# Kernel tuning notes

Hardware: AMD Instinct MI355X
Metric: run time of the kernel (lower is better)

Reference implementation:

```python
import jax, jax.numpy as jnp
import numpy as np

H = 256       # hiddenDim
E = 300       # embDim
VOCAB = 50000
S = 1024      # number of sentences in document
L = 64        # words per sentence (chain-tree depth)
TOPIC = 100
TARGET = 5


def setup_inputs() -> dict:
    key = jax.random.key(0)
    ks = jax.random.split(key, 21)
    f32 = jnp.float32
    return {
        'sentenceInIndex': jax.random.randint(ks[0], (S, L), 0, VOCAB),
        'depTypes': jax.random.randint(ks[1], (S, L - 1), 0, 9),
        'D_T_distr': jax.random.uniform(ks[2], (TOPIC,), dtype=f32),
        'h0': jax.random.normal(ks[3], (H,), dtype=f32),
        'idx2vec': jax.random.normal(ks[4], (VOCAB, E), dtype=f32) * 0.1,
        'q': jax.random.normal(ks[5], (10, H), dtype=f32) * 0.1,
        'W': jax.random.normal(ks[6], (3 * H, E), dtype=f32) * 0.05,
        'U': jax.random.normal(ks[7], (3 * H, H), dtype=f32) * 0.05,
        'D': jax.random.normal(ks[8], (3 * H, H), dtype=f32) * 0.05,
        'b': jax.random.normal(ks[9], (3 * H,), dtype=f32) * 0.05,
        'gru_wih': jax.random.normal(ks[10], (3 * H, H), dtype=f32) * 0.05,
        'gru_whh': jax.random.normal(ks[11], (3 * H, H), dtype=f32) * 0.05,
        'gru_bih': jax.random.normal(ks[12], (3 * H,), dtype=f32) * 0.05,
        'gru_bhh': jax.random.normal(ks[13], (3 * H,), dtype=f32) * 0.05,
        'gate_W': jax.random.normal(ks[14], (2 * H, H), dtype=f32) * 0.05,
        'gate_U': jax.random.normal(ks[15], (2 * H, H), dtype=f32) * 0.05,
        'gate_b': jax.random.normal(ks[16], (2 * H,), dtype=f32) * 0.05,
        'mlp_W': jax.random.normal(ks[17], (H, TOPIC), dtype=f32) * 0.05,
        'mlp_b': jax.random.normal(ks[18], (H,), dtype=f32) * 0.05,
        'out_W': jax.random.normal(ks[19], (TARGET, H), dtype=f32) * 0.05,
        'out_b': jax.random.normal(ks[20], (TARGET,), dtype=f32) * 0.05,
    }


def reference(sentenceInIndex, depTypes, D_T_distr, h0, idx2vec, q, W, U, D, b,
              gru_wih, gru_whh, gru_bih, gru_bhh,
              gate_W, gate_U, gate_b, mlp_W, mlp_b, out_W, out_b):
    # ---- DERNN over chain-canonicalized dependency trees (vectorized over S sentences) ----
    x = idx2vec[sentenceInIndex]                        # [S, L, E] gather
    Wx = jnp.einsum('sle,ke->slk', x, W)                # [S, L, 3H]
    qe = q[depTypes]                                    # [S, L-1, H] dep-type embeddings for edges k->k+1
    Dq = jnp.einsum('slh,kh->slk', qe, D)               # [S, L-1, 3H]

    # leaf node (position L-1): q_sum = q[-1] ('leafNotion'); no child h term
    dq_leaf = D @ q[-1]                                 # [3H]
    iu_leaf = Wx[:, -1, H:] + dq_leaf[H:] + b[H:]       # [S, 2H]
    h = jnp.tanh(jax.nn.sigmoid(iu_leaf[:, :H]) * jnp.tanh(iu_leaf[:, H:]))  # [S, H]

    # internal nodes k = L-2 .. 0, single child k+1 (edge k)
    pre = Wx[:, :L - 1] + Dq + b                        # [S, L-1, 3H]
    pre_rev = jnp.swapaxes(pre[:, ::-1], 0, 1)          # [L-1, S, 3H] bottom-up order

    def tree_step(h_c, pre_k):
        tot = pre_k + h_c @ U.T                         # [S, 3H]
        f = jax.nn.sigmoid(tot[:, :H]) * h_c            # child forget gate * child h (single child => sum)
        i = jax.nn.sigmoid(tot[:, H:2 * H])
        u = jnp.tanh(tot[:, 2 * H:])
        h_n = jnp.tanh(i * u + f)
        return h_n, None

    sentenceVector, _ = jax.lax.scan(tree_step, h, pre_rev)  # [S, H] root hidden per sentence

    # ---- GRU over sentence sequence (batch 1), torch nn.GRU math ----
    def gru_step(hh, xt):
        gi = gru_wih @ xt + gru_bih                     # [3H]
        gh = gru_whh @ hh + gru_bhh
        r = jax.nn.sigmoid(gi[:H] + gh[:H])
        z = jax.nn.sigmoid(gi[H:2 * H] + gh[H:2 * H])
        n = jnp.tanh(gi[2 * H:] + r * gh[2 * H:])
        return (1.0 - z) * n + z * hh, None

    hT, _ = jax.lax.scan(gru_step, h0, sentenceVector)  # [H] final hidden state

    # ---- topic vector, GATE fusion, classifier ----
    t = jnp.tanh(mlp_W @ D_T_distr + mlp_b)             # [H]
    g = gate_W @ hT + gate_U @ t + gate_b               # [2H]
    v = jnp.tanh(jax.nn.sigmoid(g[:H]) * hT + jax.nn.sigmoid(g[H:]) * t)
    return jax.nn.softmax(out_W @ v + out_b)            # [TARGET]
```

## Files before the change

kernel.cpp:

```cpp
#include <hip/hip_runtime.h>

typedef short short8 __attribute__((ext_vector_type(8)));
typedef float f4 __attribute__((ext_vector_type(4)));
typedef int i4 __attribute__((ext_vector_type(4)));
typedef _Float16 half8 __attribute__((ext_vector_type(8)));
typedef _Float16 h2 __attribute__((ext_vector_type(2)));

#define HD 256
#define ED 300
#define EP 320
#define TH 768
#define NS 1024
#define LW 64
#define SH 4.5f

__device__ __forceinline__ unsigned short f2bf(float f) {
    unsigned int u = __float_as_uint(f);
    u = (u + 0x7FFFu + ((u >> 16) & 1u)) >> 16;
    return (unsigned short)u;
}
__device__ __forceinline__ float bf2f(unsigned short s) {
    return __uint_as_float(((unsigned int)s) << 16);
}
__device__ __forceinline__ float sigm(float x) {
    return __builtin_amdgcn_rcpf(1.f + __expf(-x));
}
__device__ __forceinline__ float tanh_(float x) {
    x = fminf(fmaxf(x, -15.f), 15.f);
    return 1.f - 2.f * __builtin_amdgcn_rcpf(1.f + __expf(2.f * x));
}
__device__ __forceinline__ unsigned int pack_h2(float a, float b) {
    h2 p; p.x = (_Float16)a; p.y = (_Float16)b;
    return __builtin_bit_cast(unsigned int, p);
}

__device__ __forceinline__ void load8bf(const unsigned short* p, float* o) {
    uint4 a = *(const uint4*)p;
    o[0] = bf2f((unsigned short)(a.x & 0xffff)); o[1] = bf2f((unsigned short)(a.x >> 16));
    o[2] = bf2f((unsigned short)(a.y & 0xffff)); o[3] = bf2f((unsigned short)(a.y >> 16));
    o[4] = bf2f((unsigned short)(a.z & 0xffff)); o[5] = bf2f((unsigned short)(a.z >> 16));
    o[6] = bf2f((unsigned short)(a.w & 0xffff)); o[7] = bf2f((unsigned short)(a.w >> 16));
}
__device__ __forceinline__ void ubf4(uint2 a, float* o) {
    o[0] = bf2f((unsigned short)(a.x & 0xffff)); o[1] = bf2f((unsigned short)(a.x >> 16));
    o[2] = bf2f((unsigned short)(a.y & 0xffff)); o[3] = bf2f((unsigned short)(a.y >> 16));
}

__global__ void k_prep(const float* __restrict__ W, const float* __restrict__ U,
                       const float* __restrict__ Wih, const float* __restrict__ Whh,
                       const float* __restrict__ q, const float* __restrict__ Dm,
                       const float* __restrict__ DT, const float* __restrict__ mlpW,
                       const float* __restrict__ mlpb,
                       const float* __restrict__ bih, const float* __restrict__ bhh,
                       unsigned short* __restrict__ Wb, _Float16* __restrict__ Uh,
                       _Float16* __restrict__ Wihh,
                       signed char* __restrict__ Wq, float* __restrict__ rowscale,
                       float* __restrict__ bias2,
                       float* __restrict__ Dq, float* __restrict__ tv) {
    __shared__ float smax[4];
    int bid = blockIdx.x, tid = threadIdx.x;
    if (bid < 768) {
        int r = bid;
        for (int j = tid; j < EP; j += 256)
            Wb[r * EP + j] = (j < ED) ? f2bf(W[r * ED + j]) : (unsigned short)0;
        float whv = Whh[r * HD + tid];
        for (int j = tid; j < HD; j += 256) {
            Uh[r * HD + j] = (_Float16)U[r * HD + j];
            Wihh[r * HD + j] = (_Float16)Wih[r * HD + j];
        }
        float v = fabsf(whv);
        for (int o = 32; o; o >>= 1) v = fmaxf(v, __shfl_xor(v, o));
        if ((tid & 63) == 0) smax[tid >> 6] = v;
        __syncthreads();
        float am = fmaxf(fmaxf(smax[0], smax[1]), fmaxf(smax[2], smax[3]));
        float inv = (am > 0.f) ? 127.f / am : 0.f;
        int qi = (int)rintf(whv * inv);
        qi = max(-127, min(127, qi));
        Wq[r * HD + tid] = (signed char)qi;
        if (tid == 0) rowscale[r] = (am / 127.f) * (SH / 127.f);
    } else if (bid < 798) {
        int idx = bid - 768;
        int d = idx / 3, part = idx - d * 3;
        int n = part * 256 + tid;
        float s = 0.f;
        for (int h = 0; h < HD; ++h) s += Dm[n * HD + h] * q[d * HD + h];
        Dq[d * TH + n] = s;
    } else {
        if (tid < HD) {
            float s = 0.f;
            for (int k = 0; k < 100; ++k) s += mlpW[tid * 100 + k] * DT[k];
            tv[tid] = tanh_(s + mlpb[tid]);
        }
        for (int r = tid; r < TH; r += 256)
            bias2[r] = bih[r] + ((r < 512) ? bhh[r] : 0.f);
    }
}

#define XP 328
__launch_bounds__(256, 2)
__global__ void k_phaseB(const int* __restrict__ sIdx, const int* __restrict__ depT,
                         const float* __restrict__ emb, const unsigned short* __restrict__ Wb,
                         const float* __restrict__ Dq, const float* __restrict__ bias,
                         unsigned short* __restrict__ pre) {
    __shared__ float dq_s[10 * 772];
    __shared__ float b_s[TH];
    __shared__ int dep_s[32];
    __shared__ int idx_s[32];
    __shared__ __align__(16) unsigned short xbf[32 * XP];
    __shared__ __align__(16) unsigned short tbuf[16 * 776];
    int tid = threadIdx.x;
    int c0 = blockIdx.x * 32;
    for (int i = tid; i < 10 * 768; i += 256) {
        int d = i / 768, n = i - d * 768;
        dq_s[d * 772 + n] = Dq[i];
    }
    for (int i = tid; i < TH; i += 256) b_s[i] = bias[i];
    if (tid < 32) {
        int m = c0 + tid;
        idx_s[tid] = sIdx[m];
        int l = m & 63, s = m >> 6;
        dep_s[tid] = (l == 63) ? 9 : depT[s * 63 + l];
    }
    __syncthreads();
    for (int i = tid; i < 32 * EP; i += 256) {
        int row = i / EP, col = i - row * EP;
        unsigned short v = 0;
        if (col < ED) v = f2bf(emb[(long)idx_s[row] * ED + col]);
        xbf[row * XP + col] = v;
    }
    __syncthreads();

    int lane = tid & 63;
    int w = tid >> 6;
    int quad = lane >> 4, l16 = lane & 15;

    f4 acc[2][12];
#pragma unroll
    for (int cs = 0; cs < 2; ++cs)
#pragma unroll
        for (int ms = 0; ms < 12; ++ms) acc[cs][ms] = (f4){0.f, 0.f, 0.f, 0.f};

    const unsigned short* wbase = Wb + (w * 192 + l16) * EP;

#pragma unroll
    for (int kt = 0; kt < 10; ++kt) {
        int k0 = kt * 32 + quad * 8;
        short8 bf0 = *(const short8*)&xbf[l16 * XP + k0];
        short8 bf1 = *(const short8*)&xbf[(16 + l16) * XP + k0];
#pragma unroll
        for (int ms = 0; ms < 12; ++ms) {
            short8 af = *(const short8*)(wbase + ms * 16 * EP + k0);
            acc[0][ms] = __builtin_amdgcn_mfma_f32_16x16x32_bf16(af, bf0, acc[0][ms], 0, 0, 0);
            acc[1][ms] = __builtin_amdgcn_mfma_f32_16x16x32_bf16(af, bf1, acc[1][ms], 0, 0, 0);
        }
    }

#pragma unroll
    for (int cs = 0; cs < 2; ++cs) {
        int dep = dep_s[cs * 16 + l16];
#pragma unroll
        for (int ms = 0; ms < 12; ++ms) {
            int ncol = w * 192 + ms * 16 + quad * 4;
            f4 dq4 = *(const f4*)&dq_s[dep * 772 + ncol];
            f4 b4 = *(const f4*)&b_s[ncol];
            unsigned int lo = (unsigned int)f2bf(acc[cs][ms][0] + dq4[0] + b4[0]) |
                              ((unsigned int)f2bf(acc[cs][ms][1] + dq4[1] + b4[1]) << 16);
            unsigned int hi = (unsigned int)f2bf(acc[cs][ms][2] + dq4[2] + b4[2]) |
                              ((unsigned int)f2bf(acc[cs][ms][3] + dq4[3] + b4[3]) << 16);
            uint2 v; v.x = lo; v.y = hi;
            *(uint2*)&tbuf[l16 * 776 + ncol] = v;
        }
        __syncthreads();
        for (int it = 0; it < 6; ++it) {
            int flat = it * 256 + tid;
            int row = flat / 96;
            int ch = flat - row * 96;
            uint4 v = *(const uint4*)&tbuf[row * 776 + ch * 8];
            *(uint4*)(pre + (long)(c0 + cs * 16 + row) * TH + ch * 8) = v;
        }
        __syncthreads();
    }
}

__global__ void __launch_bounds__(768) k_phaseC(
                         const unsigned short* __restrict__ pre,
                         const _Float16* __restrict__ Uh,
                         const _Float16* __restrict__ Wihh,
                         const float* __restrict__ bias2,
                         float* __restrict__ gi) {
    __shared__ __align__(16) uint4 hfr[512];
    __shared__ __align__(16) float tot[16 * 772];
    int tid = threadIdx.x;
    int lane = tid & 63, w = tid >> 6, quad = lane >> 4, l16 = lane & 15;
    int s0 = blockIdx.x * 16;

    uint4 frag[32];
    {
        const _Float16* base = Uh + (w * 64 + l16) * HD;
#pragma unroll
        for (int t = 0; t < 4; ++t)
#pragma unroll
            for (int kt = 0; kt < 8; ++kt)
                frag[t * 8 + kt] = *(const uint4*)(base + t * 16 * HD + kt * 32 + quad * 8);
    }

    int us = tid >> 5;
    int jg = tid & 31;
    int j0 = jg * 8;
    int hcell = (j0 >> 5) * 64 + 16 * ((j0 >> 3) & 3) + us;
    uint4 hcp;

    if (tid < 512) {
        const unsigned short* prow = pre + ((long)(s0 + us) * LW + 63) * TH;
        float iv[8], uv[8], hcv[8];
        load8bf(prow + 256 + j0, iv);
        load8bf(prow + 512 + j0, uv);
#pragma unroll
        for (int r = 0; r < 8; ++r) hcv[r] = tanh_(sigm(iv[r]) * tanh_(uv[r]));
        hcp.x = pack_h2(hcv[0], hcv[1]); hcp.y = pack_h2(hcv[2], hcv[3]);
        hcp.z = pack_h2(hcv[4], hcv[5]); hcp.w = pack_h2(hcv[6], hcv[7]);
        hfr[hcell] = hcp;
    }
    __syncthreads();

    int mb = w * 64 + quad * 4;

    for (int step = 0; step < 63; ++step) {
        int l = 62 - step;
        uint2 praw[6];
        if (tid < 512) {
            const unsigned short* prow = pre + ((long)(s0 + us) * LW + l) * TH;
#pragma unroll
            for (int g = 0; g < 3; ++g) {
                praw[2 * g]     = *(const uint2*)(prow + g * 256 + j0);
                praw[2 * g + 1] = *(const uint2*)(prow + g * 256 + j0 + 4);
            }
        }
        f4 a0 = (f4){0,0,0,0}, a1 = (f4){0,0,0,0}, a2 = (f4){0,0,0,0}, a3 = (f4){0,0,0,0};
#pragma unroll
        for (int kt = 0; kt < 8; ++kt) {
            half8 b = __builtin_bit_cast(half8, hfr[kt * 64 + lane]);
            a0 = __builtin_amdgcn_mfma_f32_16x16x32_f16(__builtin_bit_cast(half8, frag[kt]), b, a0, 0, 0, 0);
            a1 = __builtin_amdgcn_mfma_f32_16x16x32_f16(__builtin_bit_cast(half8, frag[8 + kt]), b, a1, 0, 0, 0);
            a2 = __builtin_amdgcn_mfma_f32_16x16x32_f16(__builtin_bit_cast(half8, frag[16 + kt]), b, a2, 0, 0, 0);
            a3 = __builtin_amdgcn_mfma_f32_16x16x32_f16(__builtin_bit_cast(half8, frag[24 + kt]), b, a3, 0, 0, 0);
        }
        float* tr = tot + l16 * 772;
        *(f4*)&tr[mb] = a0;
        *(f4*)&tr[mb + 16] = a1;
        *(f4*)&tr[mb + 32] = a2;
        *(f4*)&tr[mb + 48] = a3;
        __syncthreads();
        if (tid < 512) {
            const float* ts = tot + us * 772;
            float hcv[8];
            h2 px = __builtin_bit_cast(h2, hcp.x); h2 py = __builtin_bit_cast(h2, hcp.y);
            h2 pz = __builtin_bit_cast(h2, hcp.z); h2 pw = __builtin_bit_cast(h2, hcp.w);
            hcv[0] = (float)px.x; hcv[1] = (float)px.y; hcv[2] = (float)py.x; hcv[3] = (float)py.y;
            hcv[4] = (float)pz.x; hcv[5] = (float)pz.y; hcv[6] = (float)pw.x; hcv[7] = (float)pw.y;
#pragma unroll
            for (int hf = 0; hf < 2; ++hf) {
                int jb = j0 + hf * 4;
                float pf[4], pi_[4], pu[4];
                ubf4(praw[hf], pf);
                ubf4(praw[2 + hf], pi_);
                ubf4(praw[4 + hf], pu);
                f4 tf = *(const f4*)&ts[jb];
                f4 ti = *(const f4*)&ts[256 + jb];
                f4 tu = *(const f4*)&ts[512 + jb];
#pragma unroll
                for (int r = 0; r < 4; ++r) {
                    float ff = tf[r] + pf[r];
                    float ii = ti[r] + pi_[r];
                    float uu = tu[r] + pu[r];
                    hcv[hf * 4 + r] = tanh_(sigm(ii) * tanh_(uu) + sigm(ff) * hcv[hf * 4 + r]);
                }
            }
            hcp.x = pack_h2(hcv[0], hcv[1]); hcp.y = pack_h2(hcv[2], hcv[3]);
            hcp.z = pack_h2(hcv[4], hcv[5]); hcp.w = pack_h2(hcv[6], hcv[7]);
            hfr[hcell] = hcp;
        }
        __syncthreads();
    }

    {
        const _Float16* base = Wihh + (w * 64 + l16) * HD;
#pragma unroll
        for (int t = 0; t < 4; ++t)
#pragma unroll
            for (int kt = 0; kt < 8; ++kt)
                frag[t * 8 + kt] = *(const uint4*)(base + t * 16 * HD + kt * 32 + quad * 8);
    }
    f4 a0 = (f4){0,0,0,0}, a1 = (f4){0,0,0,0}, a2 = (f4){0,0,0,0}, a3 = (f4){0,0,0,0};
#pragma unroll
    for (int kt = 0; kt < 8; ++kt) {
        half8 b = __builtin_bit_cast(half8, hfr[kt * 64 + lane]);
        a0 = __builtin_amdgcn_mfma_f32_16x16x32_f16(__builtin_bit_cast(half8, frag[kt]), b, a0, 0, 0, 0);
        a1 = __builtin_amdgcn_mfma_f32_16x16x32_f16(__builtin_bit_cast(half8, frag[8 + kt]), b, a1, 0, 0, 0);
        a2 = __builtin_amdgcn_mfma_f32_16x16x32_f16(__builtin_bit_cast(half8, frag[16 + kt]), b, a2, 0, 0, 0);
        a3 = __builtin_amdgcn_mfma_f32_16x16x32_f16(__builtin_bit_cast(half8, frag[24 + kt]), b, a3, 0, 0, 0);
    }
    float* go = gi + (long)(s0 + l16) * TH;
    f4 b0 = *(const f4*)(bias2 + mb);
    f4 b1 = *(const f4*)(bias2 + mb + 16);
    f4 b2 = *(const f4*)(bias2 + mb + 32);
    f4 b3 = *(const f4*)(bias2 + mb + 48);
    *(f4*)(go + mb) = a0 + b0;
    *(f4*)(go + mb + 16) = a1 + b1;
    *(f4*)(go + mb + 32) = a2 + b2;
    *(f4*)(go + mb + 48) = a3 + b3;
}

#define GB 8
__global__ void __launch_bounds__(512) k_gru(
                      const signed char* __restrict__ Wq, const float* __restrict__ rowscale,
                      const float* __restrict__ bhh,
                      const float* __restrict__ gi, const float* __restrict__ h0,
                      const float* __restrict__ tv,
                      const float* __restrict__ gateW, const float* __restrict__ gateU,
                      const float* __restrict__ gateb,
                      const float* __restrict__ outW, const float* __restrict__ outb,
                      float* __restrict__ out) {
    __shared__ __align__(16) signed char qbuf[2][HD];
    __shared__ __align__(16) float gbuf[2][GB * TH];
    __shared__ float hts[HD];
    __shared__ float sgs[512];
    __shared__ float vvs[HD];
    __shared__ float lg[8];

    int tid = threadIdx.x;
    int lane = tid & 63, w = tid >> 6, quad = lane >> 4, l16 = lane & 15;

    i4 far_[2][4], faz[2][4], fan[2][4];
#pragma unroll
    for (int c = 0; c < 2; ++c) {
        const signed char* qr_ = Wq + (long)(w * 32 + c * 16 + l16) * HD;
        const signed char* qz_ = Wq + (long)(256 + w * 32 + c * 16 + l16) * HD;
        const signed char* qn_ = Wq + (long)(512 + w * 32 + c * 16 + l16) * HD;
#pragma unroll
        for (int kc = 0; kc < 4; ++kc) {
            far_[c][kc] = *(const i4*)(qr_ + kc * 64 + quad * 16);
            faz[c][kc] = *(const i4*)(qz_ + kc * 64 + quad * 16);
            fan[c][kc] = *(const i4*)(qn_ + kc * 64 + quad * 16);
        }
    }

    int sc = (l16 >> 2) & 1;
    int sr = l16 & 3;
    int j = w * 32 + sc * 16 + quad * 4 + sr;
    bool b2 = (sr & 2) != 0, b1 = (sr & 1) != 0, bc = (sc != 0);
    bool owner = (l16 < 8);

    float rs_r = rowscale[j];
    float rs_z = rowscale[256 + j];
    float rs_n = rowscale[512 + j];
    float bn_l = bhh[512 + j];

    float hv = h0[j];
    if (owner) {
        float hc = fminf(fmaxf(hv, -SH), SH);
        qbuf[0][j] = (signed char)(int)rintf(hc * (127.f / SH));
    }
    float rg[12];
#pragma unroll
    for (int i = 0; i < 12; ++i) gbuf[0][i * 512 + tid] = gi[i * 512 + tid];
#pragma unroll
    for (int i = 0; i < 12; ++i) rg[i] = gi[GB * TH + i * 512 + tid];
    __syncthreads();

    for (int nb = 0; nb < NS / GB; ++nb) {
        int buf = nb & 1;
#pragma unroll
        for (int u = 0; u < GB; ++u) {
            if (u == 0) {
#pragma unroll
                for (int i = 0; i < 12; ++i) gbuf[buf ^ 1][i * 512 + tid] = rg[i];
                if (nb + 2 < NS / GB) {
                    const float* gsrc = gi + (long)(nb + 2) * GB * TH;
#pragma unroll
                    for (int i = 0; i < 12; ++i) rg[i] = gsrc[i * 512 + tid];
                }
            }
            const int p = u & 1;
            const float* gl = &gbuf[buf][u * TH];
            float gr_l = gl[j], gz_l = gl[256 + j], gn_l = gl[512 + j];

            i4 qr[2], qz[2], qn[2];
#pragma unroll
            for (int c = 0; c < 2; ++c) { qr[c] = (i4){0,0,0,0}; qz[c] = (i4){0,0,0,0}; qn[c] = (i4){0,0,0,0}; }
#pragma unroll
            for (int kc = 0; kc < 4; ++kc) {
                i4 b = *(const i4*)&qbuf[p][kc * 64 + quad * 16];
                qr[0] = __builtin_amdgcn_mfma_i32_16x16x64_i8(far_[0][kc], b, qr[0], 0, 0, 0);
                qr[1] = __builtin_amdgcn_mfma_i32_16x16x64_i8(far_[1][kc], b, qr[1], 0, 0, 0);
                qz[0] = __builtin_amdgcn_mfma_i32_16x16x64_i8(faz[0][kc], b, qz[0], 0, 0, 0);
                qz[1] = __builtin_amdgcn_mfma_i32_16x16x64_i8(faz[1][kc], b, qz[1], 0, 0, 0);
                qn[0] = __builtin_amdgcn_mfma_i32_16x16x64_i8(fan[0][kc], b, qn[0], 0, 0, 0);
                qn[1] = __builtin_amdgcn_mfma_i32_16x16x64_i8(fan[1][kc], b, qn[1], 0, 0, 0);
            }
            int ra0 = bc ? qr[1][0] : qr[0][0], ra1 = bc ? qr[1][1] : qr[0][1];
            int ra2 = bc ? qr[1][2] : qr[0][2], ra3 = bc ? qr[1][3] : qr[0][3];
            int rt0 = b2 ? ra2 : ra0, rt1 = b2 ? ra3 : ra1;
            int qrv = b1 ? rt1 : rt0;
            int za0 = bc ? qz[1][0] : qz[0][0], za1 = bc ? qz[1][1] : qz[0][1];
            int za2 = bc ? qz[1][2] : qz[0][2], za3 = bc ? qz[1][3] : qz[0][3];
            int zt0 = b2 ? za2 : za0, zt1 = b2 ? za3 : za1;
            int qzv = b1 ? zt1 : zt0;
            int na0 = bc ? qn[1][0] : qn[0][0], na1 = bc ? qn[1][1] : qn[0][1];
            int na2 = bc ? qn[1][2] : qn[0][2], na3 = bc ? qn[1][3] : qn[0][3];
            int nt0 = b2 ? na2 : na0, nt1 = b2 ? na3 : na1;
            int qnv = b1 ? nt1 : nt0;
            float rv = sigm(gr_l + (float)qrv * rs_r);
            float zv = sigm(gz_l + (float)qzv * rs_z);
            float nv = tanh_(gn_l + rv * ((float)qnv * rs_n + bn_l));
            hv = (1.f - zv) * nv + zv * hv;
            if (owner) {
                float hc = fminf(fmaxf(hv, -SH), SH);
                qbuf[p ^ 1][j] = (signed char)(int)rintf(hc * (127.f / SH));
            }
            __syncthreads();
        }
    }

    if (owner) hts[j] = hv;
    __syncthreads();
    {
        float s = gateb[tid];
        for (int k = 0; k < HD; ++k)
            s += gateW[tid * HD + k] * hts[k] + gateU[tid * HD + k] * tv[k];
        sgs[tid] = sigm(s);
    }
    __syncthreads();
    if (tid < HD) vvs[tid] = tanh_(sgs[tid] * hts[tid] + sgs[256 + tid] * tv[tid]);
    __syncthreads();
    if (tid < 5) {
        float s = outb[tid];
        for (int k = 0; k < HD; ++k) s += outW[tid * HD + k] * vvs[k];
        lg[tid] = s;
    }
    __syncthreads();
    if (tid == 0) {
        float m = lg[0];
        for (int i = 1; i < 5; ++i) m = fmaxf(m, lg[i]);
        float e[5], sum = 0.f;
        for (int i = 0; i < 5; ++i) { e[i] = __expf(lg[i] - m); sum += e[i]; }
        for (int i = 0; i < 5; ++i) out[i] = e[i] / sum;
    }
}

extern "C" void kernel_launch(void* const* d_in, const int* in_sizes, int n_in,
                              void* d_out, int out_size, void* d_ws, size_t ws_size,
                              hipStream_t stream) {
    (void)in_sizes; (void)n_in; (void)out_size; (void)ws_size;
    const int* sIdx = (const int*)d_in[0];
    const int* depT = (const int*)d_in[1];
    const float* DT = (const float*)d_in[2];
    const float* h0 = (const float*)d_in[3];
    const float* emb = (const float*)d_in[4];
    const float* q = (const float*)d_in[5];
    const float* W = (const float*)d_in[6];
    const float* U = (const float*)d_in[7];
    const float* Dm = (const float*)d_in[8];
    const float* b = (const float*)d_in[9];
    const float* Wih = (const float*)d_in[10];
    const float* Whh = (const float*)d_in[11];
    const float* bih = (const float*)d_in[12];
    const float* bhh = (const float*)d_in[13];
    const float* gateW = (const float*)d_in[14];
    const float* gateU = (const float*)d_in[15];
    const float* gateb = (const float*)d_in[16];
    const float* mlpW = (const float*)d_in[17];
    const float* mlpb = (const float*)d_in[18];
    const float* outW = (const float*)d_in[19];
    const float* outb = (const float*)d_in[20];

    char* ws = (char*)d_ws;
    unsigned short* Wb = (unsigned short*)ws;   ws += 768 * 320 * 2;
    _Float16* Uh = (_Float16*)ws;               ws += 768 * 256 * 2;
    _Float16* Wihh = (_Float16*)ws;             ws += 768 * 256 * 2;
    signed char* Wq = (signed char*)ws;         ws += 768 * 256;
    float* rowscale = (float*)ws;               ws += 768 * 4;
    float* bias2 = (float*)ws;                  ws += 768 * 4;
    float* Dq = (float*)ws;                     ws += 10 * 768 * 4;
    float* tv = (float*)ws;                     ws += 1024;
    ws = (char*)d_ws + ((((size_t)(ws - (char*)d_ws)) + 4095) & ~(size_t)4095);
    unsigned short* pre = (unsigned short*)ws;  ws += (size_t)65536 * 768 * 2;
    float* gi = (float*)ws;                     ws += (size_t)1024 * 768 * 4;

    k_prep<<<dim3(799), dim3(256), 0, stream>>>(W, U, Wih, Whh, q, Dm, DT, mlpW, mlpb,
                                                bih, bhh,
                                                Wb, Uh, Wihh, Wq, rowscale, bias2, Dq, tv);
    k_phaseB<<<dim3(2048), dim3(256), 0, stream>>>(sIdx, depT, emb, Wb, Dq, b, pre);
    k_phaseC<<<dim3(64), dim3(768), 0, stream>>>(pre, Uh, Wihh, bias2, gi);
    k_gru<<<dim3(1), dim3(512), 0, stream>>>(Wq, rowscale, bhh, gi, h0, tv,
                                             gateW, gateU, gateb, outW, outb, (float*)d_out);
}
```

Baseline: 1.207 ms.

## Pin GRU int8 weights in AGPRs via inline asm and split GRU launch

The recurrent int8 weight fragments are moved into accumulation registers, and the MFMA is issued through inline asm with AGPR operands. This is meant to cut VGPR pressure and avoid spills or register copies in the serial GRU loop. The 1024-step GRU is also split into two single-block launches of 512 steps each, with the hidden state passed through global memory. That adds launch overhead and still runs strictly serially. A bug remains: the prefetch guard `nb+2 < NS/GB` still reads `gi` past the first half's boundary, which is harmless but wasteful.

After: 1.357 ms. +12.4%, slower.

```diff
diff --git a/kernel.cpp b/kernel.cpp
--- a/kernel.cpp
+++ b/kernel.cpp
@@ -44,6 +44,16 @@
 __device__ __forceinline__ void ubf4(uint2 a, float* o) {
     o[0] = bf2f((unsigned short)(a.x & 0xffff)); o[1] = bf2f((unsigned short)(a.x >> 16));
     o[2] = bf2f((unsigned short)(a.y & 0xffff)); o[3] = bf2f((unsigned short)(a.y >> 16));
+}
+
+__device__ __forceinline__ i4 to_a(i4 v) {
+    i4 r;
+    asm("" : "=a"(r) : "0"(v));
+    return r;
+}
+__device__ __forceinline__ void mfma_i8_acc(i4& acc, i4 a, i4 b) {
+    asm volatile("v_mfma_i32_16x16x64_i8 %0, %1, %2, %0"
+                 : "+a"(acc) : "a"(a), "v"(b));
 }
 
 __global__ void k_prep(const float* __restrict__ W, const float* __restrict__ U,
@@ -320,7 +330,8 @@
                       const float* __restrict__ gateW, const float* __restrict__ gateU,
                       const float* __restrict__ gateb,
                       const float* __restrict__ outW, const float* __restrict__ outb,
-                      float* __restrict__ out) {
+                      float* __restrict__ out,
+                      float* __restrict__ hstate, int t0, int do_head) {
     __shared__ __align__(16) signed char qbuf[2][HD];
     __shared__ __align__(16) float gbuf[2][GB * TH];
     __shared__ float hts[HD];
@@ -339,9 +350,9 @@
         const signed char* qn_ = Wq + (long)(512 + w * 32 + c * 16 + l16) * HD;
 #pragma unroll
         for (int kc = 0; kc < 4; ++kc) {
-            far_[c][kc] = *(const i4*)(qr_ + kc * 64 + quad * 16);
-            faz[c][kc] = *(const i4*)(qz_ + kc * 64 + quad * 16);
-            fan[c][kc] = *(const i4*)(qn_ + kc * 64 + quad * 16);
+            far_[c][kc] = to_a(*(const i4*)(qr_ + kc * 64 + quad * 16));
+            faz[c][kc] = to_a(*(const i4*)(qz_ + kc * 64 + quad * 16));
+            fan[c][kc] = to_a(*(const i4*)(qn_ + kc * 64 + quad * 16));
         }
     }
 
@@ -356,20 +367,26 @@
     float rs_n = rowscale[512 + j];
     float bn_l = bhh[512 + j];
 
-    float hv = h0[j];
+    float hv = (t0 == 0) ? h0[j] : hstate[j];
     if (owner) {
         float hc = fminf(fmaxf(hv, -SH), SH);
         qbuf[0][j] = (signed char)(int)rintf(hc * (127.f / SH));
     }
+    const int nb0 = t0 / GB;
     float rg[12];
-#pragma unroll
-    for (int i = 0; i < 12; ++i) gbuf[0][i * 512 + tid] = gi[i * 512 + tid];
-#pragma unroll
-    for (int i = 0; i < 12; ++i) rg[i] = gi[GB * TH + i * 512 + tid];
-    __syncthreads();
-
-    for (int nb = 0; nb < NS / GB; ++nb) {
-        int buf = nb & 1;
+    {
+        const float* g0 = gi + (long)nb0 * GB * TH;
+        const float* g1 = gi + (long)(nb0 + 1) * GB * TH;
+#pragma unroll
+        for (int i = 0; i < 12; ++i) gbuf[0][i * 512 + tid] = g0[i * 512 + tid];
+#pragma unroll
+        for (int i = 0; i < 12; ++i) rg[i] = g1[i * 512 + tid];
+    }
+    __syncthreads();
+
+    for (int nbr = 0; nbr < 512 / GB; ++nbr) {
+        int nb = nb0 + nbr;
+        int buf = nbr & 1;
 #pragma unroll
         for (int u = 0; u < GB; ++u) {
             if (u == 0) {
@@ -391,12 +408,12 @@
 #pragma unroll
             for (int kc = 0; kc < 4; ++kc) {
                 i4 b = *(const i4*)&qbuf[p][kc * 64 + quad * 16];
-                qr[0] = __builtin_amdgcn_mfma_i32_16x16x64_i8(far_[0][kc], b, qr[0], 0, 0, 0);
-                qr[1] = __builtin_amdgcn_mfma_i32_16x16x64_i8(far_[1][kc], b, qr[1], 0, 0, 0);
-                qz[0] = __builtin_amdgcn_mfma_i32_16x16x64_i8(faz[0][kc], b, qz[0], 0, 0, 0);
-                qz[1] = __builtin_amdgcn_mfma_i32_16x16x64_i8(faz[1][kc], b, qz[1], 0, 0, 0);
-                qn[0] = __builtin_amdgcn_mfma_i32_16x16x64_i8(fan[0][kc], b, qn[0], 0, 0, 0);
-                qn[1] = __builtin_amdgcn_mfma_i32_16x16x64_i8(fan[1][kc], b, qn[1], 0, 0, 0);
+                mfma_i8_acc(qr[0], far_[0][kc], b);
+                mfma_i8_acc(qr[1], far_[1][kc], b);
+                mfma_i8_acc(qz[0], faz[0][kc], b);
+                mfma_i8_acc(qz[1], faz[1][kc], b);
+                mfma_i8_acc(qn[0], fan[0][kc], b);
+                mfma_i8_acc(qn[1], fan[1][kc], b);
             }
             int ra0 = bc ? qr[1][0] : qr[0][0], ra1 = bc ? qr[1][1] : qr[0][1];
             int ra2 = bc ? qr[1][2] : qr[0][2], ra3 = bc ? qr[1][3] : qr[0][3];
@@ -420,6 +437,11 @@
             }
             __syncthreads();
         }
+    }
+
+    if (!do_head) {
+        if (owner) hstate[j] = hv;
+        return;
     }
 
     if (owner) hts[j] = hv;
@@ -483,6 +505,7 @@
     float* bias2 = (float*)ws;                  ws += 768 * 4;
     float* Dq = (float*)ws;                     ws += 10 * 768 * 4;
     float* tv = (float*)ws;                     ws += 1024;
+    float* hstate = (float*)ws;                 ws += 1024;
     ws = (char*)d_ws + ((((size_t)(ws - (char*)d_ws)) + 4095) & ~(size_t)4095);
     unsigned short* pre = (unsigned short*)ws;  ws += (size_t)65536 * 768 * 2;
     float* gi = (float*)ws;                     ws += (size_t)1024 * 768 * 4;
@@ -493,5 +516,9 @@
     k_phaseB<<<dim3(2048), dim3(256), 0, stream>>>(sIdx, depT, emb, Wb, Dq, b, pre);
     k_phaseC<<<dim3(64), dim3(768), 0, stream>>>(pre, Uh, Wihh, bias2, gi);
     k_gru<<<dim3(1), dim3(512), 0, stream>>>(Wq, rowscale, bhh, gi, h0, tv,
-                                             gateW, gateU, gateb, outW, outb, (float*)d_out);
-}
+                                             gateW, gateU, gateb, outW, outb, (float*)d_out,
+                                             hstate, 0, 0);
+    k_gru<<<dim3(1), dim3(512), 0, stream>>>(Wq, rowscale, bhh, gi, h0, tv,
+                                             gateW, gateU, gateb, outW, outb, (float*)d_out,
+                                             hstate, 512, 1);
+}
```
